# Kernel optimization log

Hardware: AMD Instinct MI355X
Metric: run time of the kernel (lower is better)

## Reference

```python
import jax, jax.numpy as jnp
import numpy as np
import math

B = 4096
D = 768
HID = 256
C_OLD = 100
C_NEW = 100
NUM_CLASSES = 200
EPSILON = 0.05
TAU = 0.1
EPS = 1e-8
NEG_INF = -1e9


def _l2_normalize(x):
    # matches F.normalize(p=2, dim=1, eps=1e-12)
    n = jnp.linalg.norm(x, axis=1, keepdims=True)
    return x / jnp.maximum(n, 1e-12)


def setup_inputs() -> dict:
    key = jax.random.key(0)
    k1, k2, k3, k4, k5, k6, k7 = jax.random.split(key, 7)
    z_u = jax.random.normal(k1, (B, D), dtype=jnp.float32)
    logits = jax.random.normal(k2, (B, NUM_CLASSES), dtype=jnp.float32)
    old_class_indices = jnp.arange(C_OLD, dtype=jnp.int64 if jax.config.jax_enable_x64 else jnp.int32)
    new_class_indices = jnp.arange(C_OLD, C_OLD + C_NEW, dtype=old_class_indices.dtype)
    base_features = jax.random.normal(k3, (B, D), dtype=jnp.float32)
    s = 1.0 / math.sqrt(D)
    f1_w = jax.random.uniform(k4, (HID, D), dtype=jnp.float32, minval=-s, maxval=s)
    f1_b = jax.random.uniform(k5, (HID,), dtype=jnp.float32, minval=-s, maxval=s)
    f2_w = jax.random.uniform(k6, (HID, D), dtype=jnp.float32, minval=-s, maxval=s)
    f2_b = jax.random.uniform(k7, (HID,), dtype=jnp.float32, minval=-s, maxval=s)
    return {"z_u": z_u, "logits": logits, "old_class_indices": old_class_indices,
            "new_class_indices": new_class_indices, "base_features": base_features,
            "f1_w": f1_w, "f1_b": f1_b, "f2_w": f2_w, "f2_b": f2_b}


def reference(z_u, logits, old_class_indices, new_class_indices, base_features,
              f1_w, f1_b, f2_w, f2_b):
    num_old = old_class_indices.shape[0]
    active = jnp.concatenate([old_class_indices, new_class_indices])

    # ---- soft entropy regularization ----
    probs = jax.nn.softmax(logits[:, active], axis=1)   # (B, C_old+C_new)
    mean_probs = probs.mean(axis=0)
    p_old = mean_probs[:num_old].sum()
    p_new = mean_probs[num_old:].sum()
    loss_inter = (p_old * jnp.log(p_old + EPS) + p_new * jnp.log(p_new + EPS)
                  + math.log(2.0))
    p_old_in = mean_probs[:num_old] / (p_old + EPS)
    loss_old_in = jnp.sum(p_old_in * jnp.log(p_old_in + EPS)) + math.log(num_old)
    p_new_in = mean_probs[num_old:] / (p_new + EPS)
    num_new = new_class_indices.shape[0]
    if num_new > 1:
        loss_new_in = jnp.sum(p_new_in * jnp.log(p_new_in + EPS)) + math.log(num_new)
    else:
        loss_new_in = jnp.float32(0.0)
    loss_entropy = loss_inter + loss_old_in + loss_new_in

    # ---- neighborhood mask from frozen base features ----
    base_norm = _l2_normalize(base_features)
    base_sim = base_norm @ base_norm.T                  # (B, B)
    eye = jnp.eye(base_sim.shape[0], dtype=bool)
    mask = (base_sim > EPSILON) & ~eye                  # (B, B) bool

    # ---- contrastive similarities ----
    z_norm = _l2_normalize(z_u)
    sim = z_norm @ z_norm.T                             # (B, B)

    f1_z = z_u @ f1_w.T + f1_b                          # (B, HID)
    f2_z = z_u @ f2_w.T + f2_b
    attn_logits = jnp.where(mask, f1_z @ f2_z.T, NEG_INF)
    w_ik = jax.nn.softmax(attn_logits, axis=1) * mask.astype(sim.dtype)

    exp_sim = jnp.where(eye, 0.0, jnp.exp(sim / TAU))
    denom = exp_sim.sum(axis=1, keepdims=True)
    log_prob = sim / TAU - jnp.log(denom + EPS)

    num_neighbors = mask.sum(axis=1).astype(sim.dtype)  # (B,)
    valid = num_neighbors > 0
    loss_i = -(w_ik * mask.astype(sim.dtype) * log_prob).sum(axis=1)
    per_sample = jnp.where(valid, loss_i / jnp.maximum(num_neighbors, 1.0), 0.0)
    n_valid = valid.sum().astype(sim.dtype)
    loss_contrastive = jnp.where(n_valid > 0,
                                 per_sample.sum() / jnp.maximum(n_valid, 1.0),
                                 0.0)

    total_loss = loss_entropy + loss_contrastive
    return total_loss
```

## Files before the change

### kernel.cpp

```cpp
#include <hip/hip_runtime.h>
#include <hip/hip_fp8.h>


#define B_N   4096
#define D_N   768
#define HID_N 256
#define NCLS  200

typedef __attribute__((ext_vector_type(8))) short v8s;
typedef __attribute__((ext_vector_type(4))) float v4f;

__device__ __forceinline__ unsigned short f2bf(float x) {
    unsigned int u = __float_as_uint(x);
    unsigned int r = (u + 0x7FFFu + ((u >> 16) & 1u)) >> 16;
    return (unsigned short)r;
}
__device__ __forceinline__ float bf2f(unsigned short h) {
    return __uint_as_float((unsigned int)h << 16);
}
__device__ __forceinline__ unsigned char f2fp8(float x) {
    __hip_fp8_e4m3 v(x);
    return (unsigned char)v.__x;
}

__device__ __forceinline__ void gld16(const unsigned short* g, unsigned short* l) {
    __builtin_amdgcn_global_load_lds(
        (__attribute__((address_space(1))) void*)g,
        (__attribute__((address_space(3))) void*)l, 16, 0, 0);
}
__device__ __forceinline__ void gld16c(const unsigned char* g, unsigned char* l) {
    __builtin_amdgcn_global_load_lds(
        (__attribute__((address_space(1))) void*)g,
        (__attribute__((address_space(3))) void*)l, 16, 0, 0);
}

#define ZERO_ACC(a) { _Pragma("unroll") for (int _i = 0; _i < 4; _i++) \
    _Pragma("unroll") for (int _j = 0; _j < 4; _j++) a[_i][_j] = (v4f){0.f,0.f,0.f,0.f}; }

__global__ __launch_bounds__(256) void normalize_k(
    const float* __restrict__ z, const float* __restrict__ base,
    const float* __restrict__ w1, const float* __restrict__ w2,
    unsigned char* __restrict__ zn8, unsigned char* __restrict__ bn8,
    unsigned short* __restrict__ zb,
    unsigned short* __restrict__ o1, unsigned short* __restrict__ o2)
{
    int tid = threadIdx.x;
    if (blockIdx.x >= B_N) {
        int b2 = blockIdx.x - B_N;
        const float* src = (b2 < 4) ? w1 : w2;
        unsigned short* dst = (b2 < 4) ? o1 : o2;
        int base2 = (b2 & 3) * 49152 + tid;
        #pragma unroll 4
        for (int i = 0; i < 192; i++) dst[base2 + i * 256] = f2bf(src[base2 + i * 256]);
        return;
    }
    int row = blockIdx.x;
    __shared__ float ws1[4], ws2[4];
    const float* zr = z    + (size_t)row * D_N;
    const float* br = base + (size_t)row * D_N;
    float z0 = zr[tid], z1 = zr[tid + 256], z2 = zr[tid + 512];
    float b0 = br[tid], b1 = br[tid + 256], b2 = br[tid + 512];
    float s1 = z0*z0 + z1*z1 + z2*z2;
    float s2 = b0*b0 + b1*b1 + b2*b2;
    #pragma unroll
    for (int m = 32; m > 0; m >>= 1) { s1 += __shfl_xor(s1, m); s2 += __shfl_xor(s2, m); }
    if ((tid & 63) == 0) { ws1[tid >> 6] = s1; ws2[tid >> 6] = s2; }
    __syncthreads();
    float t1 = ws1[0] + ws1[1] + ws1[2] + ws1[3];
    float t2 = ws2[0] + ws2[1] + ws2[2] + ws2[3];
    float sc1 = 16.0f / fmaxf(sqrtf(t1), 1e-12f);
    float sc2 = 16.0f / fmaxf(sqrtf(t2), 1e-12f);
    size_t o = (size_t)row * D_N;
    int sw8 = ((row >> 3) & 1) << 3;
    int j0 = tid ^ sw8;
    zn8[o+j0] = f2fp8(z0*sc1); zn8[o+j0+256] = f2fp8(z1*sc1); zn8[o+j0+512] = f2fp8(z2*sc1);
    bn8[o+j0] = f2fp8(b0*sc2); bn8[o+j0+256] = f2fp8(b1*sc2); bn8[o+j0+512] = f2fp8(b2*sc2);
    zb[o+tid] = f2bf(z0);      zb[o+tid+256] = f2bf(z1);      zb[o+tid+512] = f2bf(z2);
}

__device__ __forceinline__ void mm_tile128(
    const unsigned short* __restrict__ Ag, const unsigned short* __restrict__ Bg,
    int aRow0, int bRow0, int K,
    unsigned short* Al, unsigned short* Bl, v4f acc[4][4])
{
    const int tid = threadIdx.x;
    const int lane = tid & 63, wave = tid >> 6, quad = lane >> 4, col = lane & 15;
    const int wr = wave >> 1, wc = wave & 1;
    const int r8 = lane >> 3;
    const int kbl = (lane & 7) ^ r8;
    const int sw  = col & 7;
    for (int kc = 0; kc < K; kc += 64) {
        __syncthreads();
        #pragma unroll
        for (int s = 0; s < 4; s++) {
            int rowbase = s * 32 + wave * 8;
            gld16(Ag + (size_t)(aRow0 + rowbase + r8) * K + kc + kbl * 8,
                  Al + rowbase * 64);
            gld16(Bg + (size_t)(bRow0 + rowbase + r8) * K + kc + kbl * 8,
                  Bl + rowbase * 64);
        }
        __syncthreads();
        #pragma unroll
        for (int kk = 0; kk < 2; kk++) {
            int ko = (((kk << 2) + quad) ^ sw) << 3;
            v8s af[4], bf[4];
            #pragma unroll
            for (int t = 0; t < 4; t++) {
                af[t] = *(const v8s*)(Al + (wr * 64 + t * 16 + col) * 64 + ko);
                bf[t] = *(const v8s*)(Bl + (wc * 64 + t * 16 + col) * 64 + ko);
            }
            #pragma unroll
            for (int tr = 0; tr < 4; tr++)
                #pragma unroll
                for (int tc = 0; tc < 4; tc++)
                    acc[tr][tc] = __builtin_amdgcn_mfma_f32_16x16x32_bf16(
                        af[tr], bf[tc], acc[tr][tc], 0, 0, 0);
        }
    }
}

__global__ __launch_bounds__(256, 2) void fz_gemm(
    const unsigned short* __restrict__ zb,
    const unsigned short* __restrict__ w1b, const unsigned short* __restrict__ w2b,
    const float* __restrict__ b1, const float* __restrict__ b2,
    unsigned char* __restrict__ f1z8, unsigned char* __restrict__ f2z8)
{
    __shared__ __align__(16) unsigned short Al[128 * 64];
    __shared__ __align__(16) unsigned short Bl[128 * 64];
    int which = blockIdx.y >> 1;
    const unsigned short* wb = which ? w2b : w1b;
    const float* bias = which ? b2 : b1;
    unsigned char* outz = which ? f2z8 : f1z8;
    int mBase = blockIdx.x * 128, nBase = (blockIdx.y & 1) * 128;
    v4f acc[4][4]; ZERO_ACC(acc);
    mm_tile128(zb, wb, mBase, nBase, D_N, Al, Bl, acc);
    int tid = threadIdx.x, lane = tid & 63, wave = tid >> 6, quad = lane >> 4, col = lane & 15;
    int wr = wave >> 1, wc = wave & 1;
    #pragma unroll
    for (int tr = 0; tr < 4; tr++)
        #pragma unroll
        for (int tc = 0; tc < 4; tc++) {
            int gcol = nBase + wc * 64 + tc * 16 + col;
            float bv = bias[gcol];
            #pragma unroll
            for (int reg = 0; reg < 4; reg++) {
                int grow = mBase + wr * 64 + tr * 16 + quad * 4 + reg;
                int sw8 = ((grow >> 3) & 1) << 3;
                outz[(size_t)grow * HID_N + (gcol ^ sw8)] =
                    f2fp8(4.0f * (acc[tr][tc][reg] + bv));
            }
        }
}

__global__ __launch_bounds__(256) void softmax_mean(
    const float* __restrict__ logits, const int* __restrict__ oldi,
    const int* __restrict__ newi, float* __restrict__ mpart)
{
    __shared__ int act[256];
    __shared__ float accs[4][256];
    int tid = threadIdx.x, lane = tid & 63, wave = tid >> 6;
    if (tid < NCLS) act[tid] = (tid < 100) ? oldi[tid] : newi[tid - 100];
    accs[0][tid] = 0.f; accs[1][tid] = 0.f; accs[2][tid] = 0.f; accs[3][tid] = 0.f;
    __syncthreads();
    int a0 = act[lane], a1 = act[lane + 64], a2 = act[lane + 128];
    int a3 = (lane < 8) ? act[lane + 192] : 0;
    int r0 = blockIdx.x * 16 + wave * 4;
    float c0 = 0.f, c1 = 0.f, c2 = 0.f, c3 = 0.f;
    for (int i = 0; i < 4; i++) {
        const float* lr = logits + (size_t)(r0 + i) * NCLS;
        float x0 = lr[a0], x1 = lr[a1], x2 = lr[a2];
        float x3 = (lane < 8) ? lr[a3] : -3.0e38f;
        float m = fmaxf(fmaxf(x0, x1), fmaxf(x2, x3));
        #pragma unroll
        for (int s = 32; s > 0; s >>= 1) m = fmaxf(m, __shfl_xor(m, s));
        float e0 = __expf(x0 - m), e1 = __expf(x1 - m), e2 = __expf(x2 - m);
        float e3 = (lane < 8) ? __expf(x3 - m) : 0.f;
        float sm = e0 + e1 + e2 + e3;
        #pragma unroll
        for (int s = 32; s > 0; s >>= 1) sm += __shfl_xor(sm, s);
        float inv = 1.0f / sm;
        c0 += e0 * inv; c1 += e1 * inv; c2 += e2 * inv; c3 += e3 * inv;
    }
    accs[wave][lane] = c0; accs[wave][lane + 64] = c1; accs[wave][lane + 128] = c2;
    if (lane < 8) accs[wave][lane + 192] = c3;
    __syncthreads();
    mpart[(size_t)tid * 256 + blockIdx.x] =
        accs[0][tid] + accs[1][tid] + accs[2][tid] + accs[3][tid];
}

__global__ __launch_bounds__(256, 2) void main_fused(
    const unsigned char* __restrict__ zn8, const unsigned char* __restrict__ bn8,
    const unsigned char* __restrict__ f1z8, const unsigned char* __restrict__ f2z8,
    float* __restrict__ partials)
{
    __shared__ __align__(16) unsigned char S[4 * 128 * 128];
    unsigned char* S0 = S;
    unsigned char* S1 = S + 1 * 128 * 128;
    unsigned char* S2 = S + 2 * 128 * 128;
    unsigned char* S3 = S + 3 * 128 * 128;
    int tid = threadIdx.x, lane = tid & 63, wave = tid >> 6, quad = lane >> 4, col = lane & 15;
    int wr = wave >> 1, wc = wave & 1;
    int ib = blockIdx.x, jc = blockIdx.y;
    int rBase = ib * 128 + wr * 64;
    int cBase = jc * 128 + wc * 64;
    const int r8 = lane >> 3;
    const int kbl8 = (lane & 7) ^ r8;
    const int sub8 = ((quad & 1) ^ (col >> 3)) << 3;

    v4f accB[4][4], accS[4][4];
    ZERO_ACC(accB); ZERO_ACC(accS);
    for (int kc = 0; kc < D_N; kc += 128) {
        __syncthreads();
        #pragma unroll
        for (int s = 0; s < 4; s++) {
            int rowbase = s * 32 + wave * 8;
            size_t rOff = (size_t)(ib * 128 + rowbase + r8) * D_N + kc + kbl8 * 16;
            size_t cOff = (size_t)(jc * 128 + rowbase + r8) * D_N + kc + kbl8 * 16;
            gld16c(bn8 + rOff, S0 + rowbase * 128);
            gld16c(bn8 + cOff, S1 + rowbase * 128);
            gld16c(zn8 + rOff, S2 + rowbase * 128);
            gld16c(zn8 + cOff, S3 + rowbase * 128);
        }
        __syncthreads();
        #pragma unroll
        for (int kk = 0; kk < 4; kk++) {
            int gbase = kk * 2 + (quad >> 1);
            int off = ((gbase ^ (col & 7)) << 4) + sub8;
            long a1[4], b1[4], a2[4], b2[4];
            #pragma unroll
            for (int t = 0; t < 4; t++) {
                int rA = (wr * 64 + t * 16 + col) * 128;
                int rB = (wc * 64 + t * 16 + col) * 128;
                a1[t] = *(const long*)(S0 + rA + off);
                b1[t] = *(const long*)(S1 + rB + off);
                a2[t] = *(const long*)(S2 + rA + off);
                b2[t] = *(const long*)(S3 + rB + off);
            }
            #pragma unroll
            for (int tr = 0; tr < 4; tr++)
                #pragma unroll
                for (int tc = 0; tc < 4; tc++) {
                    accB[tr][tc] = __builtin_amdgcn_mfma_f32_16x16x32_fp8_fp8(
                        a1[tr], b1[tc], accB[tr][tc], 0, 0, 0);
                    accS[tr][tc] = __builtin_amdgcn_mfma_f32_16x16x32_fp8_fp8(
                        a2[tr], b2[tc], accS[tr][tc], 0, 0, 0);
                }
        }
    }

    unsigned char* F1 = S0;
    unsigned char* F2 = S0 + 32768;
    __syncthreads();
    {
        int r4 = lane >> 4;
        #pragma unroll
        for (int s = 0; s < 8; s++) {
            int rowbase = s * 16 + wave * 4;
            int row = rowbase + r4;
            int kb = (lane & 15) ^ (row & 15);
            gld16c(f1z8 + (size_t)(ib * 128 + row) * HID_N + kb * 16, F1 + rowbase * 256);
            gld16c(f2z8 + (size_t)(jc * 128 + row) * HID_N + kb * 16, F2 + rowbase * 256);
        }
    }

    unsigned long long mb = 0ull;
    #pragma unroll
    for (int tr = 0; tr < 4; tr++)
        #pragma unroll
        for (int tc = 0; tc < 4; tc++)
            #pragma unroll
            for (int reg = 0; reg < 4; reg++) {
                int grow = rBase + tr * 16 + quad * 4 + reg;
                int gcol = cBase + tc * 16 + col;
                if (accB[tr][tc][reg] > 12.8f && grow != gcol)
                    mb |= 1ull << (tr * 16 + tc * 4 + reg);
            }

    float dsum[16];
    #pragma unroll
    for (int i = 0; i < 16; i++) dsum[i] = 0.f;
    unsigned int svp[4][4][2];
    #pragma unroll
    for (int tr = 0; tr < 4; tr++)
        #pragma unroll
        for (int tc = 0; tc < 4; tc++) {
            float s0 = accS[tr][tc][0] * 0.00390625f;
            float s1 = accS[tr][tc][1] * 0.00390625f;
            float s2 = accS[tr][tc][2] * 0.00390625f;
            float s3 = accS[tr][tc][3] * 0.00390625f;
            float svv[4] = {s0, s1, s2, s3};
            #pragma unroll
            for (int reg = 0; reg < 4; reg++) {
                int grow = rBase + tr * 16 + quad * 4 + reg;
                int gcol = cBase + tc * 16 + col;
                if (grow != gcol) dsum[tr * 4 + reg] += __expf(svv[reg] * 10.0f);
            }
            svp[tr][tc][0] = ((unsigned int)f2bf(s1) << 16) | f2bf(s0);
            svp[tr][tc][1] = ((unsigned int)f2bf(s3) << 16) | f2bf(s2);
        }

    v4f accA[4][4]; ZERO_ACC(accA);
    __syncthreads();
    #pragma unroll
    for (int kk = 0; kk < 8; kk++) {
        int gbase = kk * 2 + (quad >> 1);
        int off = ((gbase ^ col) << 4) + sub8;
        long af[4], bf[4];
        #pragma unroll
        for (int t = 0; t < 4; t++) {
            af[t] = *(const long*)(F1 + (wr * 64 + t * 16 + col) * 256 + off);
            bf[t] = *(const long*)(F2 + (wc * 64 + t * 16 + col) * 256 + off);
        }
        #pragma unroll
        for (int tr = 0; tr < 4; tr++)
            #pragma unroll
            for (int tc = 0; tc < 4; tc++)
                accA[tr][tc] = __builtin_amdgcn_mfma_f32_16x16x32_fp8_fp8(
                    af[tr], bf[tc], accA[tr][tc], 0, 0, 0);
    }

    float lsum[16], asum[16], nnf[16];
    #pragma unroll
    for (int i = 0; i < 16; i++) { lsum[i] = 0.f; asum[i] = 0.f; nnf[i] = 0.f; }
    #pragma unroll
    for (int tr = 0; tr < 4; tr++)
        #pragma unroll
        for (int tc = 0; tc < 4; tc++)
            #pragma unroll
            for (int reg = 0; reg < 4; reg++) {
                if ((mb >> (tr * 16 + tc * 4 + reg)) & 1ull) {
                    int slot = tr * 4 + reg;
                    float e = __expf(accA[tr][tc][reg] * 0.0625f);
                    unsigned int pk = svp[tr][tc][reg >> 1];
                    float sv = bf2f((unsigned short)((reg & 1) ? (pk >> 16) : (pk & 0xFFFF)));
                    lsum[slot] += e;
                    asum[slot] += e * sv;
                    nnf[slot] += 1.f;
                }
            }

    #pragma unroll
    for (int i = 0; i < 16; i++) {
        #pragma unroll
        for (int m = 1; m < 16; m <<= 1) {
            lsum[i] += __shfl_xor(lsum[i], m);
            asum[i] += __shfl_xor(asum[i], m);
            dsum[i] += __shfl_xor(dsum[i], m);
            nnf[i]  += __shfl_xor(nnf[i], m);
        }
        if (col == 0) {
            int row = rBase + (i >> 2) * 16 + quad * 4 + (i & 3);
            float4 v; v.x = lsum[i]; v.y = asum[i]; v.z = dsum[i]; v.w = nnf[i];
            *(float4*)(partials + ((size_t)row * 64 + jc * 2 + wc) * 4) = v;
        }
    }
}

__global__ __launch_bounds__(256) void row_reduce_fin(
    const float* __restrict__ partials, const float* __restrict__ mpart,
    float* __restrict__ acc, float* __restrict__ out)
{
    int tid = threadIdx.x;
    int row = blockIdx.x * 64 + (tid >> 2);
    int sub = tid & 3;
    const float4* p = (const float4*)partials + (size_t)row * 64 + sub * 16;
    float L = 0.f, A = 0.f, Dn = 0.f, NN = 0.f;
    #pragma unroll
    for (int c = 0; c < 16; c++) { float4 v = p[c]; L += v.x; A += v.y; Dn += v.z; NN += v.w; }
    #pragma unroll
    for (int m = 1; m < 4; m <<= 1) {
        L += __shfl_xor(L, m); A += __shfl_xor(A, m);
        Dn += __shfl_xor(Dn, m); NN += __shfl_xor(NN, m);
    }
    float per = 0.f, val = 0.f;
    if (sub == 0 && NN > 0.5f) {
        per = (logf(Dn + 1e-8f) - 10.0f * (A / L)) / NN;
        val = 1.0f;
    }
    __shared__ float red[256];
    __shared__ float r2s[256];
    __shared__ int amLast;
    red[tid] = per; r2s[tid] = val; __syncthreads();
    for (int s = 128; s > 0; s >>= 1) {
        if (tid < s) { red[tid] += red[tid + s]; r2s[tid] += r2s[tid + s]; }
        __syncthreads();
    }
    if (tid == 0) {
        atomicAdd(&acc[0], red[0]);
        atomicAdd(&acc[1], r2s[0]);
        __threadfence();
        int old = atomicAdd((int*)&acc[2], 1);
        amLast = (old == (int)gridDim.x - 1);
    }
    __syncthreads();
    if (!amLast) return;

    __shared__ float bcast[2];
    float pcl = 0.0f;
    if (tid < NCLS) {
        const float4* mp = (const float4*)(mpart + (size_t)tid * 256);
        float s = 0.f;
        #pragma unroll
        for (int c = 0; c < 64; c++) { float4 v = mp[c]; s += v.x + v.y + v.z + v.w; }
        pcl = s * (1.0f / 4096.0f);
    }
    red[tid] = (tid < 100) ? pcl : 0.0f; __syncthreads();
    for (int s = 128; s > 0; s >>= 1) { if (tid < s) red[tid] += red[tid + s]; __syncthreads(); }
    if (tid == 0) bcast[0] = red[0];
    __syncthreads();
    red[tid] = (tid >= 100 && tid < NCLS) ? pcl : 0.0f; __syncthreads();
    for (int s = 128; s > 0; s >>= 1) { if (tid < s) red[tid] += red[tid + s]; __syncthreads(); }
    if (tid == 0) bcast[1] = red[0];
    __syncthreads();
    float p_old = bcast[0], p_new = bcast[1];

    float t = 0.0f;
    if (tid < 100)       { float q = pcl / (p_old + 1e-8f); t = q * logf(q + 1e-8f); }
    else if (tid < NCLS) { float q = pcl / (p_new + 1e-8f); t = q * logf(q + 1e-8f); }
    red[tid] = t; __syncthreads();
    for (int s = 128; s > 0; s >>= 1) { if (tid < s) red[tid] += red[tid + s]; __syncthreads(); }

    if (tid == 0) {
        float s0 = __hip_atomic_load(&acc[0], __ATOMIC_RELAXED, __HIP_MEMORY_SCOPE_AGENT);
        float s1 = __hip_atomic_load(&acc[1], __ATOMIC_RELAXED, __HIP_MEMORY_SCOPE_AGENT);
        float loss_inter = p_old * logf(p_old + 1e-8f) + p_new * logf(p_new + 1e-8f)
                           + 0.69314718056f;
        float loss_entropy = loss_inter + red[0] + 2.0f * 4.60517018599f;
        float lc = (s1 > 0.5f) ? s0 / s1 : 0.0f;
        out[0] = loss_entropy + lc;
    }
}

extern "C" void kernel_launch(void* const* d_in, const int* in_sizes, int n_in,
                              void* d_out, int out_size, void* d_ws, size_t ws_size,
                              hipStream_t stream)
{
    const float* z_u    = (const float*)d_in[0];
    const float* logits = (const float*)d_in[1];
    const int*   oldi   = (const int*)d_in[2];
    const int*   newi   = (const int*)d_in[3];
    const float* basef  = (const float*)d_in[4];
    const float* f1w    = (const float*)d_in[5];
    const float* f1b    = (const float*)d_in[6];
    const float* f2w    = (const float*)d_in[7];
    const float* f2b    = (const float*)d_in[8];
    float* out = (float*)d_out;

    unsigned char* zn8   = (unsigned char*)d_ws;
    unsigned char* bn8   = zn8 + (size_t)B_N * D_N;
    unsigned short* zb   = (unsigned short*)(bn8 + (size_t)B_N * D_N);
    unsigned short* w1b  = zb  + (size_t)B_N * D_N;
    unsigned short* w2b  = w1b + (size_t)HID_N * D_N;
    unsigned char* f1z8  = (unsigned char*)(w2b + (size_t)HID_N * D_N);
    unsigned char* f2z8  = f1z8 + (size_t)B_N * HID_N;
    float* partials = (float*)(f2z8 + (size_t)B_N * HID_N);
    float* mpart    = partials + (size_t)B_N * 64 * 4;
    float* accums   = mpart + 256 * 256;

    hipMemsetAsync(accums, 0, 4 * sizeof(float), stream);

    normalize_k<<<B_N + 8, 256, 0, stream>>>(z_u, basef, f1w, f2w, zn8, bn8, zb, w1b, w2b);
    fz_gemm<<<dim3(B_N / 128, 4), 256, 0, stream>>>(zb, w1b, w2b, f1b, f2b, f1z8, f2z8);
    softmax_mean<<<256, 256, 0, stream>>>(logits, oldi, newi, mpart);
    main_fused<<<dim3(32, 32), 256, 0, stream>>>(zn8, bn8, f1z8, f2z8, partials);
    row_reduce_fin<<<64, 256, 0, stream>>>(partials, mpart, accums, out);
}
```

Before: 188.2 us.

## Fuse normalize, projection GEMM and softmax-mean into one prologue kernel

Merges the normalization kernel, the f1/f2 projection GEMM and the softmax-mean kernel into a single launch whose blocks pick their role by block index. The GEMM now reads fp32 z and weights directly and converts them to bf16 while staging into LDS, so the separate bf16 copies of z and the weights are no longer written and re-read. The accumulator memset moves into the kernel, removing a launch. The trade-off is a smaller 64x64 GEMM tile and a synchronous fp32 load-and-convert path without async LDS loads. The GEMM also reads z directly rather than depending on an earlier pass, which is what lets it run alongside the other blocks.

After: 177.4 us. 1.06x faster.

```diff
diff --git a/kernel.cpp b/kernel.cpp
--- a/kernel.cpp
+++ b/kernel.cpp
@@ -23,11 +23,6 @@
     return (unsigned char)v.__x;
 }
 
-__device__ __forceinline__ void gld16(const unsigned short* g, unsigned short* l) {
-    __builtin_amdgcn_global_load_lds(
-        (__attribute__((address_space(1))) void*)g,
-        (__attribute__((address_space(3))) void*)l, 16, 0, 0);
-}
 __device__ __forceinline__ void gld16c(const unsigned char* g, unsigned char* l) {
     __builtin_amdgcn_global_load_lds(
         (__attribute__((address_space(1))) void*)g,
@@ -37,155 +32,131 @@
 #define ZERO_ACC(a) { _Pragma("unroll") for (int _i = 0; _i < 4; _i++) \
     _Pragma("unroll") for (int _j = 0; _j < 4; _j++) a[_i][_j] = (v4f){0.f,0.f,0.f,0.f}; }
 
-__global__ __launch_bounds__(256) void normalize_k(
+__global__ __launch_bounds__(256) void pre_all(
     const float* __restrict__ z, const float* __restrict__ base,
     const float* __restrict__ w1, const float* __restrict__ w2,
+    const float* __restrict__ b1, const float* __restrict__ b2,
+    const float* __restrict__ logits, const int* __restrict__ oldi,
+    const int* __restrict__ newi,
     unsigned char* __restrict__ zn8, unsigned char* __restrict__ bn8,
-    unsigned short* __restrict__ zb,
-    unsigned short* __restrict__ o1, unsigned short* __restrict__ o2)
+    unsigned char* __restrict__ f1z8, unsigned char* __restrict__ f2z8,
+    float* __restrict__ mpart, float* __restrict__ accums)
 {
+    __shared__ __align__(16) unsigned char shmem[2 * 64 * 72 * 2];
     int tid = threadIdx.x;
-    if (blockIdx.x >= B_N) {
-        int b2 = blockIdx.x - B_N;
-        const float* src = (b2 < 4) ? w1 : w2;
-        unsigned short* dst = (b2 < 4) ? o1 : o2;
-        int base2 = (b2 & 3) * 49152 + tid;
-        #pragma unroll 4
-        for (int i = 0; i < 192; i++) dst[base2 + i * 256] = f2bf(src[base2 + i * 256]);
+
+    if (blockIdx.x < B_N) {
+        float* ws1 = (float*)shmem;
+        float* ws2 = ws1 + 4;
+        int row = blockIdx.x;
+        const float* zr = z    + (size_t)row * D_N;
+        const float* br = base + (size_t)row * D_N;
+        float z0 = zr[tid], z1 = zr[tid + 256], z2 = zr[tid + 512];
+        float b0 = br[tid], b1v = br[tid + 256], b2v = br[tid + 512];
+        float s1 = z0*z0 + z1*z1 + z2*z2;
+        float s2 = b0*b0 + b1v*b1v + b2v*b2v;
+        #pragma unroll
+        for (int m = 32; m > 0; m >>= 1) { s1 += __shfl_xor(s1, m); s2 += __shfl_xor(s2, m); }
+        if ((tid & 63) == 0) { ws1[tid >> 6] = s1; ws2[tid >> 6] = s2; }
+        __syncthreads();
+        float t1 = ws1[0] + ws1[1] + ws1[2] + ws1[3];
+        float t2 = ws2[0] + ws2[1] + ws2[2] + ws2[3];
+        float sc1 = 16.0f / fmaxf(sqrtf(t1), 1e-12f);
+        float sc2 = 16.0f / fmaxf(sqrtf(t2), 1e-12f);
+        size_t o = (size_t)row * D_N;
+        int j0 = tid ^ (((row >> 3) & 1) << 3);
+        zn8[o+j0] = f2fp8(z0*sc1);  zn8[o+j0+256] = f2fp8(z1*sc1);  zn8[o+j0+512] = f2fp8(z2*sc1);
+        bn8[o+j0] = f2fp8(b0*sc2);  bn8[o+j0+256] = f2fp8(b1v*sc2); bn8[o+j0+512] = f2fp8(b2v*sc2);
         return;
     }
-    int row = blockIdx.x;
-    __shared__ float ws1[4], ws2[4];
-    const float* zr = z    + (size_t)row * D_N;
-    const float* br = base + (size_t)row * D_N;
-    float z0 = zr[tid], z1 = zr[tid + 256], z2 = zr[tid + 512];
-    float b0 = br[tid], b1 = br[tid + 256], b2 = br[tid + 512];
-    float s1 = z0*z0 + z1*z1 + z2*z2;
-    float s2 = b0*b0 + b1*b1 + b2*b2;
-    #pragma unroll
-    for (int m = 32; m > 0; m >>= 1) { s1 += __shfl_xor(s1, m); s2 += __shfl_xor(s2, m); }
-    if ((tid & 63) == 0) { ws1[tid >> 6] = s1; ws2[tid >> 6] = s2; }
-    __syncthreads();
-    float t1 = ws1[0] + ws1[1] + ws1[2] + ws1[3];
-    float t2 = ws2[0] + ws2[1] + ws2[2] + ws2[3];
-    float sc1 = 16.0f / fmaxf(sqrtf(t1), 1e-12f);
-    float sc2 = 16.0f / fmaxf(sqrtf(t2), 1e-12f);
-    size_t o = (size_t)row * D_N;
-    int sw8 = ((row >> 3) & 1) << 3;
-    int j0 = tid ^ sw8;
-    zn8[o+j0] = f2fp8(z0*sc1); zn8[o+j0+256] = f2fp8(z1*sc1); zn8[o+j0+512] = f2fp8(z2*sc1);
-    bn8[o+j0] = f2fp8(b0*sc2); bn8[o+j0+256] = f2fp8(b1*sc2); bn8[o+j0+512] = f2fp8(b2*sc2);
-    zb[o+tid] = f2bf(z0);      zb[o+tid+256] = f2bf(z1);      zb[o+tid+512] = f2bf(z2);
-}
-
-__device__ __forceinline__ void mm_tile128(
-    const unsigned short* __restrict__ Ag, const unsigned short* __restrict__ Bg,
-    int aRow0, int bRow0, int K,
-    unsigned short* Al, unsigned short* Bl, v4f acc[4][4])
-{
-    const int tid = threadIdx.x;
-    const int lane = tid & 63, wave = tid >> 6, quad = lane >> 4, col = lane & 15;
-    const int wr = wave >> 1, wc = wave & 1;
-    const int r8 = lane >> 3;
-    const int kbl = (lane & 7) ^ r8;
-    const int sw  = col & 7;
-    for (int kc = 0; kc < K; kc += 64) {
-        __syncthreads();
-        #pragma unroll
-        for (int s = 0; s < 4; s++) {
-            int rowbase = s * 32 + wave * 8;
-            gld16(Ag + (size_t)(aRow0 + rowbase + r8) * K + kc + kbl * 8,
-                  Al + rowbase * 64);
-            gld16(Bg + (size_t)(bRow0 + rowbase + r8) * K + kc + kbl * 8,
-                  Bl + rowbase * 64);
-        }
-        __syncthreads();
-        #pragma unroll
-        for (int kk = 0; kk < 2; kk++) {
-            int ko = (((kk << 2) + quad) ^ sw) << 3;
-            v8s af[4], bf[4];
-            #pragma unroll
-            for (int t = 0; t < 4; t++) {
-                af[t] = *(const v8s*)(Al + (wr * 64 + t * 16 + col) * 64 + ko);
-                bf[t] = *(const v8s*)(Bl + (wc * 64 + t * 16 + col) * 64 + ko);
-            }
-            #pragma unroll
-            for (int tr = 0; tr < 4; tr++)
+    if (blockIdx.x < B_N + 256) {
+        int* act = (int*)shmem;
+        float* accs = (float*)(shmem + 1024);
+        int sb = blockIdx.x - B_N;
+        int lane = tid & 63, wave = tid >> 6;
+        if (sb == 0 && tid < 4) accums[tid] = 0.0f;
+        if (tid < NCLS) act[tid] = (tid < 100) ? oldi[tid] : newi[tid - 100];
+        accs[tid] = 0.f; accs[256 + tid] = 0.f; accs[512 + tid] = 0.f; accs[768 + tid] = 0.f;
+        __syncthreads();
+        int a0 = act[lane], a1 = act[lane + 64], a2 = act[lane + 128];
+        int a3 = (lane < 8) ? act[lane + 192] : 0;
+        int r0 = sb * 16 + wave * 4;
+        float c0 = 0.f, c1 = 0.f, c2 = 0.f, c3 = 0.f;
+        for (int i = 0; i < 4; i++) {
+            const float* lr = logits + (size_t)(r0 + i) * NCLS;
+            float x0 = lr[a0], x1 = lr[a1], x2 = lr[a2];
+            float x3 = (lane < 8) ? lr[a3] : -3.0e38f;
+            float m = fmaxf(fmaxf(x0, x1), fmaxf(x2, x3));
+            #pragma unroll
+            for (int s = 32; s > 0; s >>= 1) m = fmaxf(m, __shfl_xor(m, s));
+            float e0 = __expf(x0 - m), e1 = __expf(x1 - m), e2 = __expf(x2 - m);
+            float e3 = (lane < 8) ? __expf(x3 - m) : 0.f;
+            float sm = e0 + e1 + e2 + e3;
+            #pragma unroll
+            for (int s = 32; s > 0; s >>= 1) sm += __shfl_xor(sm, s);
+            float inv = 1.0f / sm;
+            c0 += e0 * inv; c1 += e1 * inv; c2 += e2 * inv; c3 += e3 * inv;
+        }
+        accs[wave * 256 + lane] = c0; accs[wave * 256 + lane + 64] = c1;
+        accs[wave * 256 + lane + 128] = c2;
+        if (lane < 8) accs[wave * 256 + lane + 192] = c3;
+        __syncthreads();
+        mpart[(size_t)tid * 256 + sb] =
+            accs[tid] + accs[256 + tid] + accs[512 + tid] + accs[768 + tid];
+        return;
+    }
+    {
+        unsigned short* Al = (unsigned short*)shmem;
+        unsigned short* Bl = Al + 64 * 72;
+        int f = blockIdx.x - (B_N + 256);
+        int which = f >> 8;
+        int t6 = f & 255;
+        int mBase = (t6 >> 2) * 64;
+        int nBase = (t6 & 3) * 64;
+        const float* wsrc = which ? w2 : w1;
+        const float* bias = which ? b2 : b1;
+        unsigned char* outz = which ? f2z8 : f1z8;
+        int lane = tid & 63, wave = tid >> 6, quad = lane >> 4, col = lane & 15;
+        v4f acc[4];
+        #pragma unroll
+        for (int i = 0; i < 4; i++) acc[i] = (v4f){0.f, 0.f, 0.f, 0.f};
+        for (int kc = 0; kc < D_N; kc += 64) {
+            __syncthreads();
+            #pragma unroll
+            for (int s = 0; s < 4; s++) {
+                int slot = s * 256 + tid;
+                int row = slot >> 4, k4 = slot & 15;
+                float4 va = *(const float4*)(z + (size_t)(mBase + row) * D_N + kc + k4 * 4);
+                float4 vb = *(const float4*)(wsrc + (size_t)(nBase + row) * D_N + kc + k4 * 4);
+                unsigned short* pa = Al + row * 72 + k4 * 4;
+                unsigned short* pb = Bl + row * 72 + k4 * 4;
+                pa[0] = f2bf(va.x); pa[1] = f2bf(va.y); pa[2] = f2bf(va.z); pa[3] = f2bf(va.w);
+                pb[0] = f2bf(vb.x); pb[1] = f2bf(vb.y); pb[2] = f2bf(vb.z); pb[3] = f2bf(vb.w);
+            }
+            __syncthreads();
+            #pragma unroll
+            for (int kk = 0; kk < 2; kk++) {
+                v8s af = *(const v8s*)(Al + (wave * 16 + col) * 72 + kk * 32 + quad * 8);
                 #pragma unroll
-                for (int tc = 0; tc < 4; tc++)
-                    acc[tr][tc] = __builtin_amdgcn_mfma_f32_16x16x32_bf16(
-                        af[tr], bf[tc], acc[tr][tc], 0, 0, 0);
-        }
-    }
-}
-
-__global__ __launch_bounds__(256, 2) void fz_gemm(
-    const unsigned short* __restrict__ zb,
-    const unsigned short* __restrict__ w1b, const unsigned short* __restrict__ w2b,
-    const float* __restrict__ b1, const float* __restrict__ b2,
-    unsigned char* __restrict__ f1z8, unsigned char* __restrict__ f2z8)
-{
-    __shared__ __align__(16) unsigned short Al[128 * 64];
-    __shared__ __align__(16) unsigned short Bl[128 * 64];
-    int which = blockIdx.y >> 1;
-    const unsigned short* wb = which ? w2b : w1b;
-    const float* bias = which ? b2 : b1;
-    unsigned char* outz = which ? f2z8 : f1z8;
-    int mBase = blockIdx.x * 128, nBase = (blockIdx.y & 1) * 128;
-    v4f acc[4][4]; ZERO_ACC(acc);
-    mm_tile128(zb, wb, mBase, nBase, D_N, Al, Bl, acc);
-    int tid = threadIdx.x, lane = tid & 63, wave = tid >> 6, quad = lane >> 4, col = lane & 15;
-    int wr = wave >> 1, wc = wave & 1;
-    #pragma unroll
-    for (int tr = 0; tr < 4; tr++)
+                for (int tc = 0; tc < 4; tc++) {
+                    v8s bf = *(const v8s*)(Bl + (tc * 16 + col) * 72 + kk * 32 + quad * 8);
+                    acc[tc] = __builtin_amdgcn_mfma_f32_16x16x32_bf16(af, bf, acc[tc], 0, 0, 0);
+                }
+            }
+        }
         #pragma unroll
         for (int tc = 0; tc < 4; tc++) {
-            int gcol = nBase + wc * 64 + tc * 16 + col;
+            int gcol = nBase + tc * 16 + col;
             float bv = bias[gcol];
             #pragma unroll
             for (int reg = 0; reg < 4; reg++) {
-                int grow = mBase + wr * 64 + tr * 16 + quad * 4 + reg;
+                int grow = mBase + wave * 16 + quad * 4 + reg;
                 int sw8 = ((grow >> 3) & 1) << 3;
                 outz[(size_t)grow * HID_N + (gcol ^ sw8)] =
-                    f2fp8(4.0f * (acc[tr][tc][reg] + bv));
-            }
-        }
-}
-
-__global__ __launch_bounds__(256) void softmax_mean(
-    const float* __restrict__ logits, const int* __restrict__ oldi,
-    const int* __restrict__ newi, float* __restrict__ mpart)
-{
-    __shared__ int act[256];
-    __shared__ float accs[4][256];
-    int tid = threadIdx.x, lane = tid & 63, wave = tid >> 6;
-    if (tid < NCLS) act[tid] = (tid < 100) ? oldi[tid] : newi[tid - 100];
-    accs[0][tid] = 0.f; accs[1][tid] = 0.f; accs[2][tid] = 0.f; accs[3][tid] = 0.f;
-    __syncthreads();
-    int a0 = act[lane], a1 = act[lane + 64], a2 = act[lane + 128];
-    int a3 = (lane < 8) ? act[lane + 192] : 0;
-    int r0 = blockIdx.x * 16 + wave * 4;
-    float c0 = 0.f, c1 = 0.f, c2 = 0.f, c3 = 0.f;
-    for (int i = 0; i < 4; i++) {
-        const float* lr = logits + (size_t)(r0 + i) * NCLS;
-        float x0 = lr[a0], x1 = lr[a1], x2 = lr[a2];
-        float x3 = (lane < 8) ? lr[a3] : -3.0e38f;
-        float m = fmaxf(fmaxf(x0, x1), fmaxf(x2, x3));
-        #pragma unroll
-        for (int s = 32; s > 0; s >>= 1) m = fmaxf(m, __shfl_xor(m, s));
-        float e0 = __expf(x0 - m), e1 = __expf(x1 - m), e2 = __expf(x2 - m);
-        float e3 = (lane < 8) ? __expf(x3 - m) : 0.f;
-        float sm = e0 + e1 + e2 + e3;
-        #pragma unroll
-        for (int s = 32; s > 0; s >>= 1) sm += __shfl_xor(sm, s);
-        float inv = 1.0f / sm;
-        c0 += e0 * inv; c1 += e1 * inv; c2 += e2 * inv; c3 += e3 * inv;
-    }
-    accs[wave][lane] = c0; accs[wave][lane + 64] = c1; accs[wave][lane + 128] = c2;
-    if (lane < 8) accs[wave][lane + 192] = c3;
-    __syncthreads();
-    mpart[(size_t)tid * 256 + blockIdx.x] =
-        accs[0][tid] + accs[1][tid] + accs[2][tid] + accs[3][tid];
+                    f2fp8(4.0f * (acc[tc][reg] + bv));
+            }
+        }
+    }
 }
 
 __global__ __launch_bounds__(256, 2) void main_fused(
@@ -448,20 +419,15 @@
 
     unsigned char* zn8   = (unsigned char*)d_ws;
     unsigned char* bn8   = zn8 + (size_t)B_N * D_N;
-    unsigned short* zb   = (unsigned short*)(bn8 + (size_t)B_N * D_N);
-    unsigned short* w1b  = zb  + (size_t)B_N * D_N;
-    unsigned short* w2b  = w1b + (size_t)HID_N * D_N;
-    unsigned char* f1z8  = (unsigned char*)(w2b + (size_t)HID_N * D_N);
+    unsigned char* f1z8  = bn8 + (size_t)B_N * D_N;
     unsigned char* f2z8  = f1z8 + (size_t)B_N * HID_N;
     float* partials = (float*)(f2z8 + (size_t)B_N * HID_N);
     float* mpart    = partials + (size_t)B_N * 64 * 4;
     float* accums   = mpart + 256 * 256;
 
-    hipMemsetAsync(accums, 0, 4 * sizeof(float), stream);
-
-    normalize_k<<<B_N + 8, 256, 0, stream>>>(z_u, basef, f1w, f2w, zn8, bn8, zb, w1b, w2b);
-    fz_gemm<<<dim3(B_N / 128, 4), 256, 0, stream>>>(zb, w1b, w2b, f1b, f2b, f1z8, f2z8);
-    softmax_mean<<<256, 256, 0, stream>>>(logits, oldi, newi, mpart);
+    pre_all<<<B_N + 256 + 512, 256, 0, stream>>>(
+        z_u, basef, f1w, f2w, f1b, f2b, logits, oldi, newi,
+        zn8, bn8, f1z8, f2z8, mpart, accums);
     main_fused<<<dim3(32, 32), 256, 0, stream>>>(zn8, bn8, f1z8, f2z8, partials);
     row_reduce_fin<<<64, 256, 0, stream>>>(partials, mpart, accums, out);
 }
```
